# Kernel optimization log

Hardware: AMD Instinct MI355X
Metric: run time of the kernel (lower is better)

## Reference

```python
import jax, jax.numpy as jnp
import numpy as np

N_NODES = 20000
N_EDGES = 40000
MAX_NB = 6
N_ATOM_FEAT = 98
N_BOND_FEAT = 13
HIDDEN = 256
DEPTH = 4
INPUT_SIZE = N_ATOM_FEAT + N_BOND_FEAT  # 111, hmess width


def setup_inputs() -> dict:
    key = jax.random.key(0)
    ks = jax.random.split(key, 10)
    fnode = jax.random.normal(ks[0], (N_NODES, N_ATOM_FEAT), jnp.float32)
    # fmess: col0/col1 are src/dst node indices stored as floats, cols 2: are bond features
    idx = jax.random.randint(ks[1], (N_EDGES, 2), 0, N_NODES).astype(jnp.float32)
    bond = jax.random.normal(ks[2], (N_EDGES, N_BOND_FEAT), jnp.float32)
    fmess = jnp.concatenate([idx, bond], axis=1)  # [E, 2 + n_bond_feat]
    agraph = jax.random.randint(ks[3], (N_NODES, MAX_NB), 0, N_EDGES)
    bgraph = jax.random.randint(ks[4], (N_EDGES, MAX_NB), 0, N_EDGES)
    s = 0.02
    W_z_w = jax.random.normal(ks[5], (HIDDEN, INPUT_SIZE + HIDDEN), jnp.float32) * s
    W_z_b = jnp.zeros((HIDDEN,), jnp.float32)
    W_r_w = jax.random.normal(ks[6], (HIDDEN, INPUT_SIZE), jnp.float32) * s  # no bias (W_r)
    U_r_w = jax.random.normal(ks[7], (HIDDEN, HIDDEN), jnp.float32) * s
    U_r_b = jnp.zeros((HIDDEN,), jnp.float32)
    W_h_w = jax.random.normal(ks[8], (HIDDEN, INPUT_SIZE + HIDDEN), jnp.float32) * s
    W_h_b = jnp.zeros((HIDDEN,), jnp.float32)
    W_o_w = jax.random.normal(ks[9], (HIDDEN, N_ATOM_FEAT + HIDDEN), jnp.float32) * s
    W_o_b = jnp.zeros((HIDDEN,), jnp.float32)
    return dict(fnode=fnode, fmess=fmess, agraph=agraph, bgraph=bgraph,
                W_z_w=W_z_w, W_z_b=W_z_b, W_r_w=W_r_w, U_r_w=U_r_w, U_r_b=U_r_b,
                W_h_w=W_h_w, W_h_b=W_h_b, W_o_w=W_o_w, W_o_b=W_o_b)


def reference(fnode, fmess, agraph, bgraph,
              W_z_w, W_z_b, W_r_w, U_r_w, U_r_b, W_h_w, W_h_b, W_o_w, W_o_b):
    # GraphFeatEncoder: gather src-node features and concat with bond features
    src = fmess[:, 0].astype(jnp.int32)
    x = jnp.concatenate([fnode[src], fmess[:, 2:]], axis=-1)  # [E, input_size]
    E = x.shape[0]
    H = W_z_b.shape[0]
    emask = jnp.ones((E, 1), x.dtype).at[0, 0].set(0.0)  # message 0 is padding
    Wr_x = (x @ W_r_w.T)[:, None, :]  # [E,1,H], constant across depth iterations
    h = jnp.zeros((E, H), x.dtype)
    # DGCNGRU: D-MPNN style GRU over directed-edge states
    for _ in range(DEPTH):
        h_nei = h[bgraph]                                   # [E, max_nb, H] gather
        sum_h = h_nei.sum(axis=1)                           # [E, H]
        z = jax.nn.sigmoid(jnp.concatenate([x, sum_h], axis=1) @ W_z_w.T + W_z_b)
        r = jax.nn.sigmoid(Wr_x + h_nei @ U_r_w.T + U_r_b)  # [E, max_nb, H]
        sum_gh = (r * h_nei).sum(axis=1)
        pre_h = jnp.tanh(jnp.concatenate([x, sum_gh], axis=1) @ W_h_w.T + W_h_b)
        h = ((1.0 - z) * sum_h + z * pre_h) * emask
    # DGCNEncoder readout: aggregate incoming edge states per atom
    nei_msg = h[agraph].sum(axis=1)                          # [N, H] gather + sum
    node_h = jax.nn.gelu(jnp.concatenate([fnode, nei_msg], axis=1) @ W_o_w.T + W_o_b,
                         approximate=False)                  # torch nn.GELU = exact erf
    nmask = jnp.ones((node_h.shape[0], 1), node_h.dtype).at[0, 0].set(0.0)  # node 0 pad
    hatom = node_h * nmask
    return hatom  # GraphFeatEncoder returns (hatom, None); hmol is always None
```

## Files before the change

### kernel.cpp

```cpp
#include <hip/hip_runtime.h>
#include <cstddef>
#include <cstdint>

typedef unsigned short u16;
typedef unsigned int   u32;
typedef __bf16  bf16x8 __attribute__((ext_vector_type(8)));
typedef float   f32x4  __attribute__((ext_vector_type(4)));

#define DEV __device__ __forceinline__

DEV float b2f(u16 u) { union { u32 i; float f; } c; c.i = ((u32)u) << 16; return c.f; }
DEV u16 f2b(float x) { union { float f; u32 i; } c; c.f = x; u32 b = c.i;
                       return (u16)((b + 0x7FFFu + ((b >> 16) & 1u)) >> 16); }
DEV float sigm(float x)  { return 1.0f / (1.0f + __expf(-x)); }
DEV float tanh_(float x) { return 1.0f - 2.0f / (1.0f + __expf(2.0f * x)); }
DEV float gelu_(float x) { return 0.5f * x * (1.0f + erff(x * 0.70710678118654752f)); }

DEV void u4tof8(uint4 v, float* f) {
    f[0] = b2f((u16)(v.x & 0xFFFF)); f[1] = b2f((u16)(v.x >> 16));
    f[2] = b2f((u16)(v.y & 0xFFFF)); f[3] = b2f((u16)(v.y >> 16));
    f[4] = b2f((u16)(v.z & 0xFFFF)); f[5] = b2f((u16)(v.z >> 16));
    f[6] = b2f((u16)(v.w & 0xFFFF)); f[7] = b2f((u16)(v.w >> 16));
}
DEV uint4 f8tou4(const float* f) {
    uint4 v;
    v.x = (u32)f2b(f[0]) | ((u32)f2b(f[1]) << 16);
    v.y = (u32)f2b(f[2]) | ((u32)f2b(f[3]) << 16);
    v.z = (u32)f2b(f[4]) | ((u32)f2b(f[5]) << 16);
    v.w = (u32)f2b(f[6]) | ((u32)f2b(f[7]) << 16);
    return v;
}

#define OB_H     0ull
#define OB_SH    20480000ull
#define OB_SGH   40960000ull
#define OB_UH    61440000ull
#define OB_BPRE  77440000ull
#define OB_BZ    81920000ull
#define OB_BH    82051072ull
#define OB_BU    82182144ull
#define OB_BOH   82313216ull
#define OB_BON   82444288ull
#define OB_PR    82509824ull
#define OB_PZ    102989824ull
#define OB_PH    123469824ull
#define WS_BYTES 143949824ull

__global__ __launch_bounds__(256) void k_repack(
    const float* __restrict__ Wz, const float* __restrict__ Wr,
    const float* __restrict__ Ur, const float* __restrict__ Wh,
    const float* __restrict__ Wo,
    u16* __restrict__ BpreT, u16* __restrict__ BzT, u16* __restrict__ BhT,
    u16* __restrict__ BuT, u16* __restrict__ BohT, u16* __restrict__ BonT) {
    int idx = blockIdx.x * 256 + threadIdx.x;
    if (idx < 98304) {
        int n = idx >> 7, k = idx & 127;
        float v = 0.0f;
        if (k < 111) {
            if (n < 256)       v = Wr[n * 111 + k];
            else if (n < 512)  v = Wz[(n - 256) * 367 + k];
            else               v = Wh[(n - 512) * 367 + k];
        }
        BpreT[idx] = f2b(v);
    }
    if (idx < 65536) {
        int n = idx >> 8, k = idx & 255;
        BzT[idx]  = f2b(Wz[n * 367 + 111 + k]);
        BhT[idx]  = f2b(Wh[n * 367 + 111 + k]);
        BuT[idx]  = f2b(Ur[n * 256 + k]);
        BohT[idx] = f2b(Wo[n * 354 + 98 + k]);
    }
    if (idx < 32768) {
        int n = idx >> 7, k = idx & 127;
        BonT[idx] = f2b(k < 98 ? Wo[n * 354 + k] : 0.0f);
    }
}

__global__ void k_build_x(const float* __restrict__ fnode,
                          const float* __restrict__ fmess, u16* __restrict__ x) {
    int e = blockIdx.x, c = threadIdx.x;
    int src = (int)fmess[(size_t)e * 15];
    float v = 0.0f;
    if (c < 98)       v = fnode[(size_t)src * 98 + c];
    else if (c < 111) v = fmess[(size_t)e * 15 + 2 + (c - 98)];
    x[(size_t)e * 128 + c] = f2b(v);
}

__global__ __launch_bounds__(256) void k_build_fb(const float* __restrict__ fnode,
                                                  u16* __restrict__ fb) {
    int idx = blockIdx.x * 256 + threadIdx.x;
    int n = idx >> 7, c = idx & 127;
    fb[idx] = f2b(c < 98 ? fnode[(size_t)n * 98 + c] : 0.0f);
}

DEV void stage128x64(const u16* __restrict__ g, size_t row0, int ld, int k0,
                     u16* s, int tid) {
    #pragma unroll
    for (int it = 0; it < 4; ++it) {
        int r = it * 32 + (tid >> 3);
        int c = (tid & 7) << 3;
        uint4 v = *(const uint4*)(g + (row0 + (size_t)r) * ld + k0 + c);
        int byte = (((r << 6) + c) << 1) ^ ((r & 7) << 4);
        *(uint4*)((char*)s + byte) = v;
    }
}

DEV void mma64(const u16* As, const u16* Bs, f32x4 acc[4][4], int wr, int wc, int lane) {
    int rb = (wr << 6) + (lane & 15);
    int cb = (wc << 6) + (lane & 15);
    int ko = (lane >> 4) << 3;
    #pragma unroll
    for (int kh = 0; kh < 2; ++kh) {
        bf16x8 a[4], b[4];
        #pragma unroll
        for (int i = 0; i < 4; ++i) {
            int ar = rb + (i << 4);
            int ab = (((ar << 6) + (kh << 5) + ko) << 1) ^ ((ar & 7) << 4);
            a[i] = *(const bf16x8*)((const char*)As + ab);
            int br = cb + (i << 4);
            int bb = (((br << 6) + (kh << 5) + ko) << 1) ^ ((br & 7) << 4);
            b[i] = *(const bf16x8*)((const char*)Bs + bb);
        }
        #pragma unroll
        for (int i = 0; i < 4; ++i)
            #pragma unroll
            for (int j = 0; j < 4; ++j)
                acc[i][j] = __builtin_amdgcn_mfma_f32_16x16x32_bf16(a[i], b[j], acc[i][j], 0, 0, 0);
    }
}

#define MG_PROLOG(NT)                                        \
    int tid = threadIdx.x, lane = tid & 63, w = tid >> 6;    \
    int wr = w >> 1, wc = w & 1;                             \
    int bm = blockIdx.x / (NT), bn = blockIdx.x % (NT);      \
    size_t m0 = (size_t)bm << 7; int n0 = bn << 7;           \
    f32x4 acc[4][4];                                         \
    { f32x4 zz = {0.f, 0.f, 0.f, 0.f};                       \
      _Pragma("unroll") for (int i = 0; i < 4; ++i)          \
      _Pragma("unroll") for (int j = 0; j < 4; ++j) acc[i][j] = zz; }

__global__ __launch_bounds__(256) void k_mg_p(
    const u16* __restrict__ A, const u16* __restrict__ BT,
    u16* __restrict__ Pr, u16* __restrict__ Pz, u16* __restrict__ Ph) {
    __shared__ u16 As[8192], Bs[8192];
    MG_PROLOG(6)
    for (int k0 = 0; k0 < 128; k0 += 64) {
        __syncthreads();
        stage128x64(A, m0, 128, k0, As, tid);
        stage128x64(BT, (size_t)n0, 128, k0, Bs, tid);
        __syncthreads();
        mma64(As, Bs, acc, wr, wc, lane);
    }
    int arr = bn >> 1;
    u16* dst = arr == 0 ? Pr : (arr == 1 ? Pz : Ph);
    int nn0 = ((bn & 1) << 7) + (wc << 6) + (lane & 15);
    int row0 = (int)m0 + (wr << 6) + ((lane >> 4) << 2);
    #pragma unroll
    for (int mi = 0; mi < 4; ++mi)
        #pragma unroll
        for (int r = 0; r < 4; ++r) {
            int m = row0 + mi * 16 + r;
            if (m >= 40000) continue;
            #pragma unroll
            for (int ni = 0; ni < 4; ++ni)
                dst[(size_t)m * 256 + nn0 + ni * 16] = f2b(acc[mi][ni][r]);
        }
}

__global__ __launch_bounds__(256) void k_mg_pn(
    const u16* __restrict__ A, const u16* __restrict__ BT, float* __restrict__ Pn) {
    __shared__ u16 As[8192], Bs[8192];
    MG_PROLOG(2)
    for (int k0 = 0; k0 < 128; k0 += 64) {
        __syncthreads();
        stage128x64(A, m0, 128, k0, As, tid);
        stage128x64(BT, (size_t)n0, 128, k0, Bs, tid);
        __syncthreads();
        mma64(As, Bs, acc, wr, wc, lane);
    }
    int nn0 = n0 + (wc << 6) + (lane & 15);
    int row0 = (int)m0 + (wr << 6) + ((lane >> 4) << 2);
    #pragma unroll
    for (int mi = 0; mi < 4; ++mi)
        #pragma unroll
        for (int r = 0; r < 4; ++r) {
            int m = row0 + mi * 16 + r;
            if (m >= 20000) continue;
            #pragma unroll
            for (int ni = 0; ni < 4; ++ni)
                Pn[(size_t)m * 256 + nn0 + ni * 16] = acc[mi][ni][r];
        }
}

__global__ __launch_bounds__(256) void k_mg_uh(
    const u16* __restrict__ A, const u16* __restrict__ BT, u16* __restrict__ C) {
    __shared__ u16 As[8192], Bs[8192];
    MG_PROLOG(2)
    for (int k0 = 0; k0 < 256; k0 += 64) {
        __syncthreads();
        stage128x64(A, m0, 256, k0, As, tid);
        stage128x64(BT, (size_t)n0, 256, k0, Bs, tid);
        __syncthreads();
        mma64(As, Bs, acc, wr, wc, lane);
    }
    int nn0 = n0 + (wc << 6) + (lane & 15);
    int row0 = (int)m0 + (wr << 6) + ((lane >> 4) << 2);
    #pragma unroll
    for (int mi = 0; mi < 4; ++mi)
        #pragma unroll
        for (int r = 0; r < 4; ++r) {
            int m = row0 + mi * 16 + r;
            if (m >= 40000) continue;
            #pragma unroll
            for (int ni = 0; ni < 4; ++ni)
                C[(size_t)m * 256 + nn0 + ni * 16] = f2b(acc[mi][ni][r]);
        }
}

__global__ __launch_bounds__(256) void k_mg_fused(
    const u16* __restrict__ sumh, const u16* __restrict__ sumgh,
    const u16* __restrict__ BzT, const u16* __restrict__ BhT,
    const u16* __restrict__ Pz, const u16* __restrict__ Ph,
    const float* __restrict__ bz, const float* __restrict__ bh,
    u16* __restrict__ h) {
    __shared__ u16 As1[8192], As2[8192], Bs1[8192], Bs2[8192];
    int tid = threadIdx.x, lane = tid & 63, w = tid >> 6;
    int wr = w >> 1, wc = w & 1;
    int bm = blockIdx.x >> 1, bn = blockIdx.x & 1;
    size_t m0 = (size_t)bm << 7; int n0 = bn << 7;
    f32x4 aZ[4][4], aH[4][4];
    { f32x4 zz = {0.f, 0.f, 0.f, 0.f};
      #pragma unroll
      for (int i = 0; i < 4; ++i)
          #pragma unroll
          for (int j = 0; j < 4; ++j) { aZ[i][j] = zz; aH[i][j] = zz; } }
    for (int k0 = 0; k0 < 256; k0 += 64) {
        __syncthreads();
        stage128x64(sumh,  m0, 256, k0, As1, tid);
        stage128x64(sumgh, m0, 256, k0, As2, tid);
        stage128x64(BzT, (size_t)n0, 256, k0, Bs1, tid);
        stage128x64(BhT, (size_t)n0, 256, k0, Bs2, tid);
        __syncthreads();
        mma64(As1, Bs1, aZ, wr, wc, lane);
        mma64(As2, Bs2, aH, wr, wc, lane);
    }
    int nn0 = n0 + (wc << 6) + (lane & 15);
    int row0 = (int)m0 + (wr << 6) + ((lane >> 4) << 2);
    float bzv[4], bhv[4];
    #pragma unroll
    for (int ni = 0; ni < 4; ++ni) { bzv[ni] = bz[nn0 + ni * 16]; bhv[ni] = bh[nn0 + ni * 16]; }
    #pragma unroll
    for (int mi = 0; mi < 4; ++mi)
        #pragma unroll
        for (int r = 0; r < 4; ++r) {
            int m = row0 + mi * 16 + r;
            if (m >= 40000) continue;
            #pragma unroll
            for (int ni = 0; ni < 4; ++ni) {
                size_t o = (size_t)m * 256 + nn0 + ni * 16;
                float z   = sigm(aZ[mi][ni][r] + b2f(Pz[o]) + bzv[ni]);
                float pre = tanh_(aH[mi][ni][r] + b2f(Ph[o]) + bhv[ni]);
                float ov  = (1.0f - z) * b2f(sumh[o]) + z * pre;
                if (m == 0) ov = 0.0f;
                h[o] = f2b(ov);
            }
        }
}

__global__ __launch_bounds__(256) void k_mg_out(
    const u16* __restrict__ A, const u16* __restrict__ BT,
    const float* __restrict__ bo, float* __restrict__ out) {
    __shared__ u16 As[8192], Bs[8192];
    MG_PROLOG(2)
    for (int k0 = 0; k0 < 256; k0 += 64) {
        __syncthreads();
        stage128x64(A, m0, 256, k0, As, tid);
        stage128x64(BT, (size_t)n0, 256, k0, Bs, tid);
        __syncthreads();
        mma64(As, Bs, acc, wr, wc, lane);
    }
    int nn0 = n0 + (wc << 6) + (lane & 15);
    int row0 = (int)m0 + (wr << 6) + ((lane >> 4) << 2);
    float bov[4];
    #pragma unroll
    for (int ni = 0; ni < 4; ++ni) bov[ni] = bo[nn0 + ni * 16];
    #pragma unroll
    for (int mi = 0; mi < 4; ++mi)
        #pragma unroll
        for (int r = 0; r < 4; ++r) {
            int m = row0 + mi * 16 + r;
            if (m >= 20000) continue;
            #pragma unroll
            for (int ni = 0; ni < 4; ++ni) {
                size_t o = (size_t)m * 256 + nn0 + ni * 16;
                float v = gelu_(acc[mi][ni][r] + out[o] + bov[ni]);
                out[o] = (m == 0) ? 0.0f : v;
            }
        }
}

__global__ __launch_bounds__(256) void k_depth1(
    const u16* __restrict__ Pz, const u16* __restrict__ Ph,
    const float* __restrict__ bz, const float* __restrict__ bh,
    u16* __restrict__ h) {
    int idx = blockIdx.x * 256 + threadIdx.x;
    int e = idx >> 5, c = (idx & 31) << 3;
    size_t o = (size_t)e * 256 + c;
    float pz[8], ph[8], r[8];
    u4tof8(*(const uint4*)(Pz + o), pz);
    u4tof8(*(const uint4*)(Ph + o), ph);
    #pragma unroll
    for (int q = 0; q < 8; ++q)
        r[q] = (e == 0) ? 0.0f : sigm(pz[q] + bz[c + q]) * tanh_(ph[q] + bh[c + q]);
    *(uint4*)(h + o) = f8tou4(r);
}

__global__ __launch_bounds__(256) void k_gather_edge(
    const u16* __restrict__ h, const u16* __restrict__ Uh,
    const u16* __restrict__ Pr, const float* __restrict__ urb,
    const int* __restrict__ bgraph,
    u16* __restrict__ sumh, u16* __restrict__ sumgh) {
    int e = (blockIdx.x << 3) + (threadIdx.x >> 5);
    int c = (threadIdx.x & 31) << 3;
    size_t o = (size_t)e * 256 + c;
    float pr[8];
    u4tof8(*(const uint4*)(Pr + o), pr);
    #pragma unroll
    for (int q = 0; q < 8; ++q) pr[q] += urb[c + q];
    float sh[8] = {}, sg[8] = {};
    #pragma unroll
    for (int j = 0; j < 6; ++j) {
        int b = bgraph[e * 6 + j];
        float hv[8], uv[8];
        u4tof8(*(const uint4*)(h  + (size_t)b * 256 + c), hv);
        u4tof8(*(const uint4*)(Uh + (size_t)b * 256 + c), uv);
        #pragma unroll
        for (int q = 0; q < 8; ++q) {
            sh[q] += hv[q];
            sg[q] += sigm(pr[q] + uv[q]) * hv[q];
        }
    }
    *(uint4*)(sumh  + o) = f8tou4(sh);
    *(uint4*)(sumgh + o) = f8tou4(sg);
}

__global__ __launch_bounds__(256) void k_gather_node(
    const u16* __restrict__ h, const int* __restrict__ agraph,
    u16* __restrict__ nei) {
    int n = (blockIdx.x << 3) + (threadIdx.x >> 5);
    int c = (threadIdx.x & 31) << 3;
    float s[8] = {};
    #pragma unroll
    for (int j = 0; j < 6; ++j) {
        int a = agraph[n * 6 + j];
        float hv[8];
        u4tof8(*(const uint4*)(h + (size_t)a * 256 + c), hv);
        #pragma unroll
        for (int q = 0; q < 8; ++q) s[q] += hv[q];
    }
    *(uint4*)(nei + (size_t)n * 256 + c) = f8tou4(s);
}

extern "C" void kernel_launch(void* const* d_in, const int* in_sizes, int n_in,
                              void* d_out, int out_size, void* d_ws, size_t ws_size,
                              hipStream_t stream) {
    if (ws_size < WS_BYTES) return;

    const float* fnode  = (const float*)d_in[0];
    const float* fmess  = (const float*)d_in[1];
    const int*   agraph = (const int*)d_in[2];
    const int*   bgraph = (const int*)d_in[3];
    const float* Wz  = (const float*)d_in[4];
    const float* bz  = (const float*)d_in[5];
    const float* Wr  = (const float*)d_in[6];
    const float* Ur  = (const float*)d_in[7];
    const float* urb = (const float*)d_in[8];
    const float* Wh  = (const float*)d_in[9];
    const float* bh  = (const float*)d_in[10];
    const float* Wo  = (const float*)d_in[11];
    const float* bo  = (const float*)d_in[12];

    char* base = (char*)d_ws;
    u16* h     = (u16*)(base + OB_H);
    u16* sumh  = (u16*)(base + OB_SH);
    u16* x     = (u16*)(base + OB_SH);
    u16* sumgh = (u16*)(base + OB_SGH);
    u16* fb    = (u16*)(base + OB_SGH);
    u16* Uh    = (u16*)(base + OB_UH);
    u16* neib  = (u16*)(base + OB_UH);
    u16* BpreT = (u16*)(base + OB_BPRE);
    u16* BzT   = (u16*)(base + OB_BZ);
    u16* BhT   = (u16*)(base + OB_BH);
    u16* BuT   = (u16*)(base + OB_BU);
    u16* BohT  = (u16*)(base + OB_BOH);
    u16* BonT  = (u16*)(base + OB_BON);
    u16* Pr    = (u16*)(base + OB_PR);
    u16* Pz    = (u16*)(base + OB_PZ);
    u16* Ph    = (u16*)(base + OB_PH);
    float* out = (float*)d_out;

    hipLaunchKernelGGL(k_repack, dim3(384), dim3(256), 0, stream,
                       Wz, Wr, Ur, Wh, Wo, BpreT, BzT, BhT, BuT, BohT, BonT);
    hipLaunchKernelGGL(k_build_x, dim3(40000), dim3(128), 0, stream, fnode, fmess, x);
    hipLaunchKernelGGL(k_build_fb, dim3(10000), dim3(256), 0, stream, fnode, fb);
    hipLaunchKernelGGL(k_mg_p,  dim3(313 * 6), dim3(256), 0, stream, x, BpreT, Pr, Pz, Ph);
    hipLaunchKernelGGL(k_mg_pn, dim3(157 * 2), dim3(256), 0, stream, fb, BonT, out);
    hipLaunchKernelGGL(k_depth1, dim3(5000), dim3(256), 0, stream, Pz, Ph, bz, bh, h);
    for (int d = 1; d < 4; ++d) {
        hipLaunchKernelGGL(k_mg_uh, dim3(313 * 2), dim3(256), 0, stream, h, BuT, Uh);
        hipLaunchKernelGGL(k_gather_edge, dim3(5000), dim3(256), 0, stream,
                           h, Uh, Pr, urb, bgraph, sumh, sumgh);
        hipLaunchKernelGGL(k_mg_fused, dim3(313 * 2), dim3(256), 0, stream,
                           sumh, sumgh, BzT, BhT, Pz, Ph, bz, bh, h);
    }
    hipLaunchKernelGGL(k_gather_node, dim3(2500), dim3(256), 0, stream, h, agraph, neib);
    hipLaunchKernelGGL(k_mg_out, dim3(157 * 2), dim3(256), 0, stream, neib, BohT, bo, out);
}
```

Before: 483.5 us.

## Recompute x-projections inside fused GEMMs instead of storing Pz/Ph/Pn

Drops the precomputed bf16 Pz/Ph buffers and the fp32 node partial. Instead the fused GRU GEMM uses K=384 over [x, sumh/sumgh], and the readout GEMM uses K=384 over [fnode, nei]. Depth 1 becomes its own GEMM kernel, the U_r bias is folded into the Pr precompute, and the MFMA operands are swapped so the epilogue can write vectorized ushort4/float4 stores. This trades extra MFMA work for less global memory traffic and fewer launches.

Result: slower. 500.3 us (+3.5%).

```diff
diff --git a/kernel.cpp b/kernel.cpp
--- a/kernel.cpp
+++ b/kernel.cpp
@@ -31,48 +31,44 @@
     return v;
 }
 
-#define OB_H     0ull
-#define OB_SH    20480000ull
-#define OB_SGH   40960000ull
-#define OB_UH    61440000ull
-#define OB_BPRE  77440000ull
-#define OB_BZ    81920000ull
-#define OB_BH    82051072ull
-#define OB_BU    82182144ull
-#define OB_BOH   82313216ull
-#define OB_BON   82444288ull
-#define OB_PR    82509824ull
-#define OB_PZ    102989824ull
-#define OB_PH    123469824ull
-#define WS_BYTES 143949824ull
+#define OB_X     0ull
+#define OB_FB    10240000ull
+#define OB_PRU   15360000ull
+#define OB_H     35840000ull
+#define OB_UH    56320000ull
+#define OB_SH    76800000ull
+#define OB_SGH   97280000ull
+#define OB_BZ    117760000ull
+#define OB_BH    117956608ull
+#define OB_BU    118153216ull
+#define OB_BR    118284288ull
+#define OB_BO    118349824ull
+#define WS_BYTES 118546432ull
 
 __global__ __launch_bounds__(256) void k_repack(
     const float* __restrict__ Wz, const float* __restrict__ Wr,
     const float* __restrict__ Ur, const float* __restrict__ Wh,
     const float* __restrict__ Wo,
-    u16* __restrict__ BpreT, u16* __restrict__ BzT, u16* __restrict__ BhT,
-    u16* __restrict__ BuT, u16* __restrict__ BohT, u16* __restrict__ BonT) {
+    u16* __restrict__ BzT, u16* __restrict__ BhT, u16* __restrict__ BuT,
+    u16* __restrict__ BrT, u16* __restrict__ BoT) {
     int idx = blockIdx.x * 256 + threadIdx.x;
-    if (idx < 98304) {
-        int n = idx >> 7, k = idx & 127;
-        float v = 0.0f;
-        if (k < 111) {
-            if (n < 256)       v = Wr[n * 111 + k];
-            else if (n < 512)  v = Wz[(n - 256) * 367 + k];
-            else               v = Wh[(n - 512) * 367 + k];
-        }
-        BpreT[idx] = f2b(v);
+    {
+        int n = idx / 384, k = idx % 384;
+        float vz, vh, vo;
+        if (k < 111)      { vz = Wz[n * 367 + k];          vh = Wh[n * 367 + k]; }
+        else if (k < 128) { vz = 0.0f;                     vh = 0.0f; }
+        else              { vz = Wz[n * 367 + k - 17];     vh = Wh[n * 367 + k - 17]; }
+        if (k < 98)       vo = Wo[n * 354 + k];
+        else if (k < 128) vo = 0.0f;
+        else              vo = Wo[n * 354 + k - 30];
+        BzT[idx] = f2b(vz); BhT[idx] = f2b(vh); BoT[idx] = f2b(vo);
     }
     if (idx < 65536) {
-        int n = idx >> 8, k = idx & 255;
-        BzT[idx]  = f2b(Wz[n * 367 + 111 + k]);
-        BhT[idx]  = f2b(Wh[n * 367 + 111 + k]);
-        BuT[idx]  = f2b(Ur[n * 256 + k]);
-        BohT[idx] = f2b(Wo[n * 354 + 98 + k]);
+        BuT[idx] = f2b(Ur[idx]);
     }
     if (idx < 32768) {
         int n = idx >> 7, k = idx & 127;
-        BonT[idx] = f2b(k < 98 ? Wo[n * 354 + k] : 0.0f);
+        BrT[idx] = f2b(k < 111 ? Wr[n * 111 + k] : 0.0f);
     }
 }
 
@@ -105,7 +101,7 @@
     }
 }
 
-DEV void mma64(const u16* As, const u16* Bs, f32x4 acc[4][4], int wr, int wc, int lane) {
+DEV void mma64s(const u16* As, const u16* Bs, f32x4 acc[4][4], int wr, int wc, int lane) {
     int rb = (wr << 6) + (lane & 15);
     int cb = (wc << 6) + (lane & 15);
     int ko = (lane >> 4) << 3;
@@ -125,208 +121,212 @@
         for (int i = 0; i < 4; ++i)
             #pragma unroll
             for (int j = 0; j < 4; ++j)
-                acc[i][j] = __builtin_amdgcn_mfma_f32_16x16x32_bf16(a[i], b[j], acc[i][j], 0, 0, 0);
-    }
-}
-
-#define MG_PROLOG(NT)                                        \
+                acc[i][j] = __builtin_amdgcn_mfma_f32_16x16x32_bf16(b[j], a[i], acc[i][j], 0, 0, 0);
+    }
+}
+
+#define MG_PROLOG()                                          \
     int tid = threadIdx.x, lane = tid & 63, w = tid >> 6;    \
     int wr = w >> 1, wc = w & 1;                             \
-    int bm = blockIdx.x / (NT), bn = blockIdx.x % (NT);      \
+    int bm = blockIdx.x >> 1, bn = blockIdx.x & 1;           \
     size_t m0 = (size_t)bm << 7; int n0 = bn << 7;           \
-    f32x4 acc[4][4];                                         \
+    int row_l = (wr << 6) + (lane & 15);                     \
+    int col_l = (wc << 6) + ((lane >> 4) << 2);
+
+#define ACC_INIT(A)                                          \
     { f32x4 zz = {0.f, 0.f, 0.f, 0.f};                       \
       _Pragma("unroll") for (int i = 0; i < 4; ++i)          \
-      _Pragma("unroll") for (int j = 0; j < 4; ++j) acc[i][j] = zz; }
+      _Pragma("unroll") for (int j = 0; j < 4; ++j) A[i][j] = zz; }
 
 __global__ __launch_bounds__(256) void k_mg_p(
-    const u16* __restrict__ A, const u16* __restrict__ BT,
-    u16* __restrict__ Pr, u16* __restrict__ Pz, u16* __restrict__ Ph) {
+    const u16* __restrict__ x, const u16* __restrict__ BrT,
+    const float* __restrict__ urb, u16* __restrict__ PrU) {
     __shared__ u16 As[8192], Bs[8192];
-    MG_PROLOG(6)
+    MG_PROLOG()
+    f32x4 acc[4][4]; ACC_INIT(acc)
     for (int k0 = 0; k0 < 128; k0 += 64) {
         __syncthreads();
-        stage128x64(A, m0, 128, k0, As, tid);
-        stage128x64(BT, (size_t)n0, 128, k0, Bs, tid);
-        __syncthreads();
-        mma64(As, Bs, acc, wr, wc, lane);
-    }
-    int arr = bn >> 1;
-    u16* dst = arr == 0 ? Pr : (arr == 1 ? Pz : Ph);
-    int nn0 = ((bn & 1) << 7) + (wc << 6) + (lane & 15);
-    int row0 = (int)m0 + (wr << 6) + ((lane >> 4) << 2);
-    #pragma unroll
-    for (int mi = 0; mi < 4; ++mi)
-        #pragma unroll
-        for (int r = 0; r < 4; ++r) {
-            int m = row0 + mi * 16 + r;
-            if (m >= 40000) continue;
-            #pragma unroll
-            for (int ni = 0; ni < 4; ++ni)
-                dst[(size_t)m * 256 + nn0 + ni * 16] = f2b(acc[mi][ni][r]);
-        }
-}
-
-__global__ __launch_bounds__(256) void k_mg_pn(
-    const u16* __restrict__ A, const u16* __restrict__ BT, float* __restrict__ Pn) {
-    __shared__ u16 As[8192], Bs[8192];
-    MG_PROLOG(2)
+        stage128x64(x, m0, 128, k0, As, tid);
+        stage128x64(BrT, (size_t)n0, 128, k0, Bs, tid);
+        __syncthreads();
+        mma64s(As, Bs, acc, wr, wc, lane);
+    }
+    #pragma unroll
+    for (int mi = 0; mi < 4; ++mi) {
+        int m = (int)m0 + row_l + (mi << 4);
+        if (m >= 40000) continue;
+        #pragma unroll
+        for (int ni = 0; ni < 4; ++ni) {
+            int col = n0 + col_l + (ni << 4);
+            float4 ub = *(const float4*)(urb + col);
+            ushort4 o;
+            o.x = f2b(acc[mi][ni][0] + ub.x); o.y = f2b(acc[mi][ni][1] + ub.y);
+            o.z = f2b(acc[mi][ni][2] + ub.z); o.w = f2b(acc[mi][ni][3] + ub.w);
+            *(ushort4*)(PrU + (size_t)m * 256 + col) = o;
+        }
+    }
+}
+
+__global__ __launch_bounds__(256) void k_d1(
+    const u16* __restrict__ x, const u16* __restrict__ BzT,
+    const u16* __restrict__ BhT, const float* __restrict__ bz,
+    const float* __restrict__ bh, u16* __restrict__ h) {
+    __shared__ u16 As[8192], Bs1[8192], Bs2[8192];
+    MG_PROLOG()
+    f32x4 aZ[4][4], aH[4][4]; ACC_INIT(aZ) ACC_INIT(aH)
     for (int k0 = 0; k0 < 128; k0 += 64) {
         __syncthreads();
-        stage128x64(A, m0, 128, k0, As, tid);
-        stage128x64(BT, (size_t)n0, 128, k0, Bs, tid);
-        __syncthreads();
-        mma64(As, Bs, acc, wr, wc, lane);
-    }
-    int nn0 = n0 + (wc << 6) + (lane & 15);
-    int row0 = (int)m0 + (wr << 6) + ((lane >> 4) << 2);
-    #pragma unroll
-    for (int mi = 0; mi < 4; ++mi)
-        #pragma unroll
-        for (int r = 0; r < 4; ++r) {
-            int m = row0 + mi * 16 + r;
-            if (m >= 20000) continue;
-            #pragma unroll
-            for (int ni = 0; ni < 4; ++ni)
-                Pn[(size_t)m * 256 + nn0 + ni * 16] = acc[mi][ni][r];
-        }
+        stage128x64(x, m0, 128, k0, As, tid);
+        stage128x64(BzT, (size_t)n0, 384, k0, Bs1, tid);
+        stage128x64(BhT, (size_t)n0, 384, k0, Bs2, tid);
+        __syncthreads();
+        mma64s(As, Bs1, aZ, wr, wc, lane);
+        mma64s(As, Bs2, aH, wr, wc, lane);
+    }
+    #pragma unroll
+    for (int mi = 0; mi < 4; ++mi) {
+        int m = (int)m0 + row_l + (mi << 4);
+        if (m >= 40000) continue;
+        #pragma unroll
+        for (int ni = 0; ni < 4; ++ni) {
+            int col = n0 + col_l + (ni << 4);
+            float4 vz = *(const float4*)(bz + col);
+            float4 vh = *(const float4*)(bh + col);
+            float r[4];
+            r[0] = sigm(aZ[mi][ni][0] + vz.x) * tanh_(aH[mi][ni][0] + vh.x);
+            r[1] = sigm(aZ[mi][ni][1] + vz.y) * tanh_(aH[mi][ni][1] + vh.y);
+            r[2] = sigm(aZ[mi][ni][2] + vz.z) * tanh_(aH[mi][ni][2] + vh.z);
+            r[3] = sigm(aZ[mi][ni][3] + vz.w) * tanh_(aH[mi][ni][3] + vh.w);
+            if (m == 0) { r[0] = r[1] = r[2] = r[3] = 0.0f; }
+            ushort4 o;
+            o.x = f2b(r[0]); o.y = f2b(r[1]); o.z = f2b(r[2]); o.w = f2b(r[3]);
+            *(ushort4*)(h + (size_t)m * 256 + col) = o;
+        }
+    }
 }
 
 __global__ __launch_bounds__(256) void k_mg_uh(
     const u16* __restrict__ A, const u16* __restrict__ BT, u16* __restrict__ C) {
     __shared__ u16 As[8192], Bs[8192];
-    MG_PROLOG(2)
+    MG_PROLOG()
+    f32x4 acc[4][4]; ACC_INIT(acc)
     for (int k0 = 0; k0 < 256; k0 += 64) {
         __syncthreads();
         stage128x64(A, m0, 256, k0, As, tid);
         stage128x64(BT, (size_t)n0, 256, k0, Bs, tid);
         __syncthreads();
-        mma64(As, Bs, acc, wr, wc, lane);
-    }
-    int nn0 = n0 + (wc << 6) + (lane & 15);
-    int row0 = (int)m0 + (wr << 6) + ((lane >> 4) << 2);
-    #pragma unroll
-    for (int mi = 0; mi < 4; ++mi)
-        #pragma unroll
-        for (int r = 0; r < 4; ++r) {
-            int m = row0 + mi * 16 + r;
-            if (m >= 40000) continue;
+        mma64s(As, Bs, acc, wr, wc, lane);
+    }
+    #pragma unroll
+    for (int mi = 0; mi < 4; ++mi) {
+        int m = (int)m0 + row_l + (mi << 4);
+        if (m >= 40000) continue;
+        #pragma unroll
+        for (int ni = 0; ni < 4; ++ni) {
+            int col = n0 + col_l + (ni << 4);
+            ushort4 o;
+            o.x = f2b(acc[mi][ni][0]); o.y = f2b(acc[mi][ni][1]);
+            o.z = f2b(acc[mi][ni][2]); o.w = f2b(acc[mi][ni][3]);
+            *(ushort4*)(C + (size_t)m * 256 + col) = o;
+        }
+    }
+}
+
+__global__ __launch_bounds__(256) void k_mg_fused(
+    const u16* __restrict__ x, const u16* __restrict__ sumh,
+    const u16* __restrict__ sumgh, const u16* __restrict__ BzT,
+    const u16* __restrict__ BhT, const float* __restrict__ bz,
+    const float* __restrict__ bh, u16* __restrict__ h) {
+    __shared__ u16 As1[8192], As2[8192], Bs1[8192], Bs2[8192];
+    MG_PROLOG()
+    f32x4 aZ[4][4], aH[4][4]; ACC_INIT(aZ) ACC_INIT(aH)
+    for (int s = 0; s < 6; ++s) {
+        int k0 = s << 6;
+        __syncthreads();
+        if (s < 2) {
+            stage128x64(x, m0, 128, k0, As1, tid);
+        } else {
+            stage128x64(sumh,  m0, 256, k0 - 128, As1, tid);
+            stage128x64(sumgh, m0, 256, k0 - 128, As2, tid);
+        }
+        stage128x64(BzT, (size_t)n0, 384, k0, Bs1, tid);
+        stage128x64(BhT, (size_t)n0, 384, k0, Bs2, tid);
+        __syncthreads();
+        mma64s(As1, Bs1, aZ, wr, wc, lane);
+        mma64s(s < 2 ? As1 : As2, Bs2, aH, wr, wc, lane);
+    }
+    #pragma unroll
+    for (int mi = 0; mi < 4; ++mi) {
+        int m = (int)m0 + row_l + (mi << 4);
+        if (m >= 40000) continue;
+        #pragma unroll
+        for (int ni = 0; ni < 4; ++ni) {
+            int col = n0 + col_l + (ni << 4);
+            float4 vz = *(const float4*)(bz + col);
+            float4 vh = *(const float4*)(bh + col);
+            ushort4 sh4 = *(const ushort4*)(sumh + (size_t)m * 256 + col);
+            float shv[4] = {b2f(sh4.x), b2f(sh4.y), b2f(sh4.z), b2f(sh4.w)};
+            float bzv[4] = {vz.x, vz.y, vz.z, vz.w};
+            float bhv[4] = {vh.x, vh.y, vh.z, vh.w};
+            float o[4];
             #pragma unroll
-            for (int ni = 0; ni < 4; ++ni)
-                C[(size_t)m * 256 + nn0 + ni * 16] = f2b(acc[mi][ni][r]);
-        }
-}
-
-__global__ __launch_bounds__(256) void k_mg_fused(
-    const u16* __restrict__ sumh, const u16* __restrict__ sumgh,
-    const u16* __restrict__ BzT, const u16* __restrict__ BhT,
-    const u16* __restrict__ Pz, const u16* __restrict__ Ph,
-    const float* __restrict__ bz, const float* __restrict__ bh,
-    u16* __restrict__ h) {
-    __shared__ u16 As1[8192], As2[8192], Bs1[8192], Bs2[8192];
-    int tid = threadIdx.x, lane = tid & 63, w = tid >> 6;
-    int wr = w >> 1, wc = w & 1;
-    int bm = blockIdx.x >> 1, bn = blockIdx.x & 1;
-    size_t m0 = (size_t)bm << 7; int n0 = bn << 7;
-    f32x4 aZ[4][4], aH[4][4];
-    { f32x4 zz = {0.f, 0.f, 0.f, 0.f};
-      #pragma unroll
-      for (int i = 0; i < 4; ++i)
-          #pragma unroll
-          for (int j = 0; j < 4; ++j) { aZ[i][j] = zz; aH[i][j] = zz; } }
-    for (int k0 = 0; k0 < 256; k0 += 64) {
-        __syncthreads();
-        stage128x64(sumh,  m0, 256, k0, As1, tid);
-        stage128x64(sumgh, m0, 256, k0, As2, tid);
-        stage128x64(BzT, (size_t)n0, 256, k0, Bs1, tid);
-        stage128x64(BhT, (size_t)n0, 256, k0, Bs2, tid);
-        __syncthreads();
-        mma64(As1, Bs1, aZ, wr, wc, lane);
-        mma64(As2, Bs2, aH, wr, wc, lane);
-    }
-    int nn0 = n0 + (wc << 6) + (lane & 15);
-    int row0 = (int)m0 + (wr << 6) + ((lane >> 4) << 2);
-    float bzv[4], bhv[4];
-    #pragma unroll
-    for (int ni = 0; ni < 4; ++ni) { bzv[ni] = bz[nn0 + ni * 16]; bhv[ni] = bh[nn0 + ni * 16]; }
-    #pragma unroll
-    for (int mi = 0; mi < 4; ++mi)
-        #pragma unroll
-        for (int r = 0; r < 4; ++r) {
-            int m = row0 + mi * 16 + r;
-            if (m >= 40000) continue;
-            #pragma unroll
-            for (int ni = 0; ni < 4; ++ni) {
-                size_t o = (size_t)m * 256 + nn0 + ni * 16;
-                float z   = sigm(aZ[mi][ni][r] + b2f(Pz[o]) + bzv[ni]);
-                float pre = tanh_(aH[mi][ni][r] + b2f(Ph[o]) + bhv[ni]);
-                float ov  = (1.0f - z) * b2f(sumh[o]) + z * pre;
-                if (m == 0) ov = 0.0f;
-                h[o] = f2b(ov);
+            for (int q = 0; q < 4; ++q) {
+                float z   = sigm(aZ[mi][ni][q] + bzv[q]);
+                float pre = tanh_(aH[mi][ni][q] + bhv[q]);
+                o[q] = (1.0f - z) * shv[q] + z * pre;
             }
-        }
+            if (m == 0) { o[0] = o[1] = o[2] = o[3] = 0.0f; }
+            ushort4 ov;
+            ov.x = f2b(o[0]); ov.y = f2b(o[1]); ov.z = f2b(o[2]); ov.w = f2b(o[3]);
+            *(ushort4*)(h + (size_t)m * 256 + col) = ov;
+        }
+    }
 }
 
 __global__ __launch_bounds__(256) void k_mg_out(
-    const u16* __restrict__ A, const u16* __restrict__ BT,
-    const float* __restrict__ bo, float* __restrict__ out) {
+    const u16* __restrict__ fb, const u16* __restrict__ nei,
+    const u16* __restrict__ BoT, const float* __restrict__ bo,
+    float* __restrict__ out) {
     __shared__ u16 As[8192], Bs[8192];
-    MG_PROLOG(2)
-    for (int k0 = 0; k0 < 256; k0 += 64) {
-        __syncthreads();
-        stage128x64(A, m0, 256, k0, As, tid);
-        stage128x64(BT, (size_t)n0, 256, k0, Bs, tid);
-        __syncthreads();
-        mma64(As, Bs, acc, wr, wc, lane);
-    }
-    int nn0 = n0 + (wc << 6) + (lane & 15);
-    int row0 = (int)m0 + (wr << 6) + ((lane >> 4) << 2);
-    float bov[4];
-    #pragma unroll
-    for (int ni = 0; ni < 4; ++ni) bov[ni] = bo[nn0 + ni * 16];
-    #pragma unroll
-    for (int mi = 0; mi < 4; ++mi)
-        #pragma unroll
-        for (int r = 0; r < 4; ++r) {
-            int m = row0 + mi * 16 + r;
-            if (m >= 20000) continue;
-            #pragma unroll
-            for (int ni = 0; ni < 4; ++ni) {
-                size_t o = (size_t)m * 256 + nn0 + ni * 16;
-                float v = gelu_(acc[mi][ni][r] + out[o] + bov[ni]);
-                out[o] = (m == 0) ? 0.0f : v;
-            }
-        }
-}
-
-__global__ __launch_bounds__(256) void k_depth1(
-    const u16* __restrict__ Pz, const u16* __restrict__ Ph,
-    const float* __restrict__ bz, const float* __restrict__ bh,
-    u16* __restrict__ h) {
-    int idx = blockIdx.x * 256 + threadIdx.x;
-    int e = idx >> 5, c = (idx & 31) << 3;
-    size_t o = (size_t)e * 256 + c;
-    float pz[8], ph[8], r[8];
-    u4tof8(*(const uint4*)(Pz + o), pz);
-    u4tof8(*(const uint4*)(Ph + o), ph);
-    #pragma unroll
-    for (int q = 0; q < 8; ++q)
-        r[q] = (e == 0) ? 0.0f : sigm(pz[q] + bz[c + q]) * tanh_(ph[q] + bh[c + q]);
-    *(uint4*)(h + o) = f8tou4(r);
+    MG_PROLOG()
+    f32x4 acc[4][4]; ACC_INIT(acc)
+    for (int s = 0; s < 6; ++s) {
+        int k0 = s << 6;
+        __syncthreads();
+        if (s < 2) stage128x64(fb,  m0, 128, k0, As, tid);
+        else       stage128x64(nei, m0, 256, k0 - 128, As, tid);
+        stage128x64(BoT, (size_t)n0, 384, k0, Bs, tid);
+        __syncthreads();
+        mma64s(As, Bs, acc, wr, wc, lane);
+    }
+    #pragma unroll
+    for (int mi = 0; mi < 4; ++mi) {
+        int m = (int)m0 + row_l + (mi << 4);
+        if (m >= 20000) continue;
+        #pragma unroll
+        for (int ni = 0; ni < 4; ++ni) {
+            int col = n0 + col_l + (ni << 4);
+            float4 vb = *(const float4*)(bo + col);
+            float4 o;
+            o.x = gelu_(acc[mi][ni][0] + vb.x);
+            o.y = gelu_(acc[mi][ni][1] + vb.y);
+            o.z = gelu_(acc[mi][ni][2] + vb.z);
+            o.w = gelu_(acc[mi][ni][3] + vb.w);
+            if (m == 0) { o.x = o.y = o.z = o.w = 0.0f; }
+            *(float4*)(out + (size_t)m * 256 + col) = o;
+        }
+    }
 }
 
 __global__ __launch_bounds__(256) void k_gather_edge(
     const u16* __restrict__ h, const u16* __restrict__ Uh,
-    const u16* __restrict__ Pr, const float* __restrict__ urb,
-    const int* __restrict__ bgraph,
+    const u16* __restrict__ PrU, const int* __restrict__ bgraph,
     u16* __restrict__ sumh, u16* __restrict__ sumgh) {
     int e = (blockIdx.x << 3) + (threadIdx.x >> 5);
     int c = (threadIdx.x & 31) << 3;
     size_t o = (size_t)e * 256 + c;
     float pr[8];
-    u4tof8(*(const uint4*)(Pr + o), pr);
-    #pragma unroll
-    for (int q = 0; q < 8; ++q) pr[q] += urb[c + q];
+    u4tof8(*(const uint4*)(PrU + o), pr);
     float sh[8] = {}, sg[8] = {};
     #pragma unroll
     for (int j = 0; j < 6; ++j) {
@@ -381,38 +381,34 @@
     const float* bo  = (const float*)d_in[12];
 
     char* base = (char*)d_ws;
+    u16* x     = (u16*)(base + OB_X);
+    u16* fb    = (u16*)(base + OB_FB);
+    u16* PrU   = (u16*)(base + OB_PRU);
     u16* h     = (u16*)(base + OB_H);
+    u16* Uh    = (u16*)(base + OB_UH);
+    u16* nei   = (u16*)(base + OB_UH);
     u16* sumh  = (u16*)(base + OB_SH);
-    u16* x     = (u16*)(base + OB_SH);
     u16* sumgh = (u16*)(base + OB_SGH);
-    u16* fb    = (u16*)(base + OB_SGH);
-    u16* Uh    = (u16*)(base + OB_UH);
-    u16* neib  = (u16*)(base + OB_UH);
-    u16* BpreT = (u16*)(base + OB_BPRE);
     u16* BzT   = (u16*)(base + OB_BZ);
     u16* BhT   = (u16*)(base + OB_BH);
     u16* BuT   = (u16*)(base + OB_BU);
-    u16* BohT  = (u16*)(base + OB_BOH);
-    u16* BonT  = (u16*)(base + OB_BON);
-    u16* Pr    = (u16*)(base + OB_PR);
-    u16* Pz    = (u16*)(base + OB_PZ);
-    u16* Ph    = (u16*)(base + OB_PH);
+    u16* BrT   = (u16*)(base + OB_BR);
+    u16* BoT   = (u16*)(base + OB_BO);
     float* out = (float*)d_out;
 
     hipLaunchKernelGGL(k_repack, dim3(384), dim3(256), 0, stream,
-                       Wz, Wr, Ur, Wh, Wo, BpreT, BzT, BhT, BuT, BohT, BonT);
+                       Wz, Wr, Ur, Wh, Wo, BzT, BhT, BuT, BrT, BoT);
     hipLaunchKernelGGL(k_build_x, dim3(40000), dim3(128), 0, stream, fnode, fmess, x);
     hipLaunchKernelGGL(k_build_fb, dim3(10000), dim3(256), 0, stream, fnode, fb);
-    hipLaunchKernelGGL(k_mg_p,  dim3(313 * 6), dim3(256), 0, stream, x, BpreT, Pr, Pz, Ph);
-    hipLaunchKernelGGL(k_mg_pn, dim3(157 * 2), dim3(256), 0, stream, fb, BonT, out);
-    hipLaunchKernelGGL(k_depth1, dim3(5000), dim3(256), 0, stream, Pz, Ph, bz, bh, h);
+    hipLaunchKernelGGL(k_mg_p, dim3(313 * 2), dim3(256), 0, stream, x, BrT, urb, PrU);
+    hipLaunchKernelGGL(k_d1,   dim3(313 * 2), dim3(256), 0, stream, x, BzT, BhT, bz, bh, h);
     for (int d = 1; d < 4; ++d) {
         hipLaunchKernelGGL(k_mg_uh, dim3(313 * 2), dim3(256), 0, stream, h, BuT, Uh);
         hipLaunchKernelGGL(k_gather_edge, dim3(5000), dim3(256), 0, stream,
-                           h, Uh, Pr, urb, bgraph, sumh, sumgh);
+                           h, Uh, PrU, bgraph, sumh, sumgh);
         hipLaunchKernelGGL(k_mg_fused, dim3(313 * 2), dim3(256), 0, stream,
-                           sumh, sumgh, BzT, BhT, Pz, Ph, bz, bh, h);
-    }
-    hipLaunchKernelGGL(k_gather_node, dim3(2500), dim3(256), 0, stream, h, agraph, neib);
-    hipLaunchKernelGGL(k_mg_out, dim3(157 * 2), dim3(256), 0, stream, neib, BohT, bo, out);
-}
+                           x, sumh, sumgh, BzT, BhT, bz, bh, h);
+    }
+    hipLaunchKernelGGL(k_gather_node, dim3(2500), dim3(256), 0, stream, h, agraph, nei);
+    hipLaunchKernelGGL(k_mg_out, dim3(157 * 2), dim3(256), 0, stream, fb, nei, BoT, bo, out);
+}
```
